# Optimization experiments

Hardware: AMD Instinct MI355X
Metric: run time of the kernel (lower is better)

## Reference

```python
import jax, jax.numpy as jnp
import numpy as np

B, K, N, F = 32, 4, 512, 128


def setup_inputs() -> dict:
    key = jax.random.key(0)
    k1, k2, k3, k4 = jax.random.split(key, 4)
    H = jax.random.normal(k1, (B, N, F), dtype=jnp.float32)
    E = jax.random.uniform(k2, (B, K, N, N), dtype=jnp.float32)
    # xavier_normal_ equivalents
    rw_std = float(np.sqrt(2.0 / (F + F * K)))  # torch xavier treats last dims
    RW = jax.random.normal(k3, (F, F, K), dtype=jnp.float32) * rw_std
    sw_std = float(np.sqrt(2.0 / (F + F)))
    SW = jax.random.normal(k4, (F, F), dtype=jnp.float32) * sw_std
    return {"H": H, "E": E, "RW": RW, "SW": SW}


def reference(H, E, RW, SW):
    # D = 1 / sum over (k, i) of (E + I)  -> [b, n]
    n = E.shape[2]
    D = 1.0 / (E + jnp.eye(n, dtype=E.dtype)).sum(axis=(1, 2))  # [b, n]
    # relational aggregation: sum_{k,j,m} E[b,k,i,j] H[b,j,m] RW[m,f,k] -> [b,i,f]
    rel = jnp.einsum('bkij,bjm,mfk->bif', E, H, RW)
    self_term = jnp.einsum('bjf,fl->bjl', H, SW)
    return jax.nn.sigmoid(D[:, :, None] * rel + self_term)
```

## Files before the change

### kernel.cpp

```cpp
#include <hip/hip_runtime.h>
#include <hip/hip_bf16.h>

#define B_ 32
#define K_ 4
#define N_ 512
#define F_ 128

typedef __attribute__((ext_vector_type(8))) short short8;
typedef __attribute__((ext_vector_type(4))) short short4v;
typedef __attribute__((ext_vector_type(4))) float float4v;

__device__ __forceinline__ unsigned short f2bf(float x) {
    unsigned int u = __builtin_bit_cast(unsigned int, x);
    u += 0x7FFFu + ((u >> 16) & 1u);
    return (unsigned short)(u >> 16);
}

__device__ __forceinline__ short8 pack8(float4v a, float4v b) {
    short8 r;
    r[0] = (short)f2bf(a[0]); r[1] = (short)f2bf(a[1]);
    r[2] = (short)f2bf(a[2]); r[3] = (short)f2bf(a[3]);
    r[4] = (short)f2bf(b[0]); r[5] = (short)f2bf(b[1]);
    r[6] = (short)f2bf(b[2]); r[7] = (short)f2bf(b[3]);
    return r;
}

__global__ void k0_weights(const float* __restrict__ RW, const float* __restrict__ SW,
                           unsigned short* __restrict__ Wt, unsigned short* __restrict__ SWt) {
    int r = blockIdx.x;
    int m = threadIdx.x;
    if (r < 512) {
        int k = r >> 7, f = r & 127;
        Wt[r * F_ + m] = f2bf(RW[(m * F_ + f) * K_ + k]);
    } else {
        int l = r - 512;
        SWt[l * F_ + m] = f2bf(SW[m * F_ + l]);
    }
}

__global__ void __launch_bounds__(256)
k1v3_convert(const float* __restrict__ E, float* __restrict__ colsum,
             unsigned short* __restrict__ Ebf) {
    int bid = blockIdx.x;
    int b   = bid >> 6;
    int k   = (bid >> 4) & 3;
    int isl = bid & 15;
    int t   = threadIdx.x;
    int j8  = (t & 63) * 8;
    int r0  = isl * 32 + (t >> 6) * 8;

    const size_t base = ((size_t)((b * K_ + k) * N_ + r0)) * N_ + j8;
    const float* Ep = E + base;
    unsigned short* Op = Ebf + base;

    float4v va[8], vb[8];
#pragma unroll
    for (int r = 0; r < 4; ++r) {
        va[r] = *(const float4v*)(Ep + (size_t)r * N_);
        vb[r] = *(const float4v*)(Ep + (size_t)r * N_ + 4);
    }
#pragma unroll
    for (int r = 4; r < 8; ++r) {
        va[r] = *(const float4v*)(Ep + (size_t)r * N_);
        vb[r] = *(const float4v*)(Ep + (size_t)r * N_ + 4);
    }

    float cs[8];
#pragma unroll
    for (int e = 0; e < 8; ++e) cs[e] = 0.f;
#pragma unroll
    for (int r = 0; r < 8; ++r) {
        cs[0] += va[r][0]; cs[1] += va[r][1]; cs[2] += va[r][2]; cs[3] += va[r][3];
        cs[4] += vb[r][0]; cs[5] += vb[r][1]; cs[6] += vb[r][2]; cs[7] += vb[r][3];
        *(short8*)(Op + (size_t)r * N_) = pack8(va[r], vb[r]);
    }

    __shared__ float red[256][9];
#pragma unroll
    for (int e = 0; e < 8; ++e) red[t][e] = cs[e];
    __syncthreads();
    if (t < 64) {
#pragma unroll
        for (int e = 0; e < 8; ++e) {
            float s = red[t][e] + red[t + 64][e] + red[t + 128][e] + red[t + 192][e];
            atomicAdd(&colsum[b * N_ + t * 8 + e], s);
        }
    }
}

__global__ void __launch_bounds__(256)
k2v2_expand(const float* __restrict__ H, const unsigned short* __restrict__ Wt,
            unsigned short* __restrict__ Tt) {
    int bid = blockIdx.x;
    int b  = bid >> 5;
    int ct = (bid >> 2) & 7;
    int jt = bid & 3;
    int lane = threadIdx.x & 63;
    int wv   = threadIdx.x >> 6;
    int c0 = ct * 64 + wv * 16;
    int jbase = jt * 128;
    int lrow = lane & 15, lgrp = lane >> 4;

    float4v acc[8];
#pragma unroll
    for (int i = 0; i < 8; ++i) acc[i] = {0.f, 0.f, 0.f, 0.f};

#pragma unroll
    for (int ms = 0; ms < 4; ++ms) {
        int m0 = ms * 32;
        short8 a = *(const short8*)(Wt + (c0 + lrow) * F_ + m0 + lgrp * 8);
        float4v hv0[8], hv1[8];
#pragma unroll
        for (int cf = 0; cf < 8; ++cf) {
            const float* hp = H + ((size_t)b * N_ + jbase + cf * 16 + lrow) * F_ + m0 + lgrp * 8;
            hv0[cf] = *(const float4v*)hp;
            hv1[cf] = *(const float4v*)(hp + 4);
        }
#pragma unroll
        for (int cf = 0; cf < 8; ++cf) {
            short8 bb = pack8(hv0[cf], hv1[cf]);
            acc[cf] = __builtin_amdgcn_mfma_f32_16x16x32_bf16(a, bb, acc[cf], 0, 0, 0);
        }
    }
#pragma unroll
    for (int cf = 0; cf < 8; ++cf) {
#pragma unroll
        for (int r = 0; r < 4; ++r) {
            int c = c0 + lgrp * 4 + r;
            int j = jbase + cf * 16 + lrow;
            Tt[((size_t)b * 512 + c) * N_ + j] = f2bf(acc[cf][r]);
        }
    }
}

__global__ void __launch_bounds__(512)
k3v3_rel(const unsigned short* __restrict__ Ebf, const unsigned short* __restrict__ Tt,
         float* __restrict__ relP) {
    int bid = blockIdx.x;
    int b  = bid >> 5;
    int it = (bid >> 2) & 7;
    int jc = bid & 3;
    int lane = threadIdx.x & 63;
    int wv   = threadIdx.x >> 6;
    int i0 = it * 64 + (wv >> 1) * 16;
    int f0 = (wv & 1) * 64;
    int lrow = lane & 15, lgrp = lane >> 4;
    int jbase = jc * 128;

    float4v acc[4];
#pragma unroll
    for (int i = 0; i < 4; ++i) acc[i] = {0.f, 0.f, 0.f, 0.f};

    const unsigned short* Eb = Ebf + ((size_t)(b * K_) * N_ + (i0 + lrow)) * N_ + jbase + lgrp * 8;
    const unsigned short* Tb = Tt + ((size_t)b * 512 + f0 + lrow) * N_ + jbase + lgrp * 8;

#define EA(t) (const short8*)(Eb + ((t) >> 2) * 262144 + ((t) & 3) * 32)
#define TA(t, cf) (const short8*)(Tb + ((t) >> 2) * 65536 + (cf) * 8192 + ((t) & 3) * 32)

    short8 a0, b00, b01, b02, b03;
    short8 a1, b10, b11, b12, b13;
    a0 = *EA(0); b00 = *TA(0, 0); b01 = *TA(0, 1); b02 = *TA(0, 2); b03 = *TA(0, 3);

    for (int t = 0; t < 16; t += 2) {
        int t1 = t + 1;
        int t2 = (t + 2 < 16) ? t + 2 : 15;
        a1 = *EA(t1); b10 = *TA(t1, 0); b11 = *TA(t1, 1); b12 = *TA(t1, 2); b13 = *TA(t1, 3);
        acc[0] = __builtin_amdgcn_mfma_f32_16x16x32_bf16(a0, b00, acc[0], 0, 0, 0);
        acc[1] = __builtin_amdgcn_mfma_f32_16x16x32_bf16(a0, b01, acc[1], 0, 0, 0);
        acc[2] = __builtin_amdgcn_mfma_f32_16x16x32_bf16(a0, b02, acc[2], 0, 0, 0);
        acc[3] = __builtin_amdgcn_mfma_f32_16x16x32_bf16(a0, b03, acc[3], 0, 0, 0);
        a0 = *EA(t2); b00 = *TA(t2, 0); b01 = *TA(t2, 1); b02 = *TA(t2, 2); b03 = *TA(t2, 3);
        acc[0] = __builtin_amdgcn_mfma_f32_16x16x32_bf16(a1, b10, acc[0], 0, 0, 0);
        acc[1] = __builtin_amdgcn_mfma_f32_16x16x32_bf16(a1, b11, acc[1], 0, 0, 0);
        acc[2] = __builtin_amdgcn_mfma_f32_16x16x32_bf16(a1, b12, acc[2], 0, 0, 0);
        acc[3] = __builtin_amdgcn_mfma_f32_16x16x32_bf16(a1, b13, acc[3], 0, 0, 0);
    }
#undef EA
#undef TA

    float* dst = relP + (size_t)jc * (B_ * N_ * F_);
#pragma unroll
    for (int cf = 0; cf < 4; ++cf) {
#pragma unroll
        for (int r = 0; r < 4; ++r) {
            int i = i0 + lgrp * 4 + r;
            int f = f0 + cf * 16 + lrow;
            dst[((size_t)b * N_ + i) * F_ + f] = acc[cf][r];
        }
    }
}

__global__ void __launch_bounds__(512)
k4_epi(const float* __restrict__ relP, const float* __restrict__ H,
       const unsigned short* __restrict__ SWt, const float* __restrict__ colsum,
       float* __restrict__ out) {
    int bid = blockIdx.x;
    int b  = bid >> 3;
    int it = bid & 7;
    int lane = threadIdx.x & 63;
    int wv   = threadIdx.x >> 6;
    int i0 = it * 64 + (wv >> 1) * 16;
    int f0 = (wv & 1) * 64;
    int lrow = lane & 15, lgrp = lane >> 4;

    float4v accS[4];
#pragma unroll
    for (int i = 0; i < 4; ++i) accS[i] = {0.f, 0.f, 0.f, 0.f};

    const float* Hp = H + ((size_t)b * N_ + i0 + lrow) * F_;
#pragma unroll
    for (int ms = 0; ms < 4; ++ms) {
        int m0 = ms * 32;
        const float* hp = Hp + m0 + lgrp * 8;
        float4v h0 = *(const float4v*)hp;
        float4v h1 = *(const float4v*)(hp + 4);
        short8 a = pack8(h0, h1);
#pragma unroll
        for (int cf = 0; cf < 4; ++cf) {
            const unsigned short* sp = SWt + (f0 + cf * 16 + lrow) * F_ + m0 + lgrp * 8;
            short8 bb = *(const short8*)sp;
            accS[cf] = __builtin_amdgcn_mfma_f32_16x16x32_bf16(a, bb, accS[cf], 0, 0, 0);
        }
    }

    float Dv[4];
#pragma unroll
    for (int r = 0; r < 4; ++r) {
        int i = i0 + lgrp * 4 + r;
        Dv[r] = 1.0f / (colsum[b * N_ + i] + (float)K_);
    }
    const size_t S = (size_t)B_ * N_ * F_;
#pragma unroll
    for (int cf = 0; cf < 4; ++cf) {
#pragma unroll
        for (int r = 0; r < 4; ++r) {
            int i = i0 + lgrp * 4 + r;
            int f = f0 + cf * 16 + lrow;
            size_t idx = ((size_t)b * N_ + i) * F_ + f;
            float v = relP[idx] + relP[idx + S] + relP[idx + 2 * S] + relP[idx + 3 * S];
            float x = Dv[r] * v + accS[cf][r];
            out[idx] = 1.0f / (1.0f + __expf(-x));
        }
    }
}

__global__ void k1_colsum(const float* __restrict__ E, float* __restrict__ colsum) {
    int bid = blockIdx.x;
    int b   = bid >> 5;
    int jt  = (bid >> 4) & 1;
    int isl = bid & 15;
    int j   = jt * 256 + threadIdx.x;
    int i0  = isl * 32;
    float s0 = 0.f, s1 = 0.f, s2 = 0.f, s3 = 0.f;
#pragma unroll
    for (int k = 0; k < K_; ++k) {
        const float* p = E + ((size_t)((b * K_ + k) * N_ + i0)) * N_ + j;
#pragma unroll 4
        for (int ii = 0; ii < 32; ii += 4) {
            s0 += p[(ii + 0) * N_];
            s1 += p[(ii + 1) * N_];
            s2 += p[(ii + 2) * N_];
            s3 += p[(ii + 3) * N_];
        }
    }
    atomicAdd(&colsum[b * N_ + j], (s0 + s1) + (s2 + s3));
}

__global__ void __launch_bounds__(512)
k3_fuse(const float* __restrict__ E, const float* __restrict__ H,
        const unsigned short* __restrict__ Tt, const unsigned short* __restrict__ SWt,
        const float* __restrict__ colsum, float* __restrict__ out) {
    int bid = blockIdx.x;
    int b  = bid >> 3;
    int it = bid & 7;
    int lane = threadIdx.x & 63;
    int wv   = threadIdx.x >> 6;
    int i0 = it * 64 + (wv >> 1) * 16;
    int f0 = (wv & 1) * 64;
    int lrow = lane & 15, lgrp = lane >> 4;

    float4v accR[4], accS[4];
#pragma unroll
    for (int i = 0; i < 4; ++i) { accR[i] = {0.f, 0.f, 0.f, 0.f}; accS[i] = {0.f, 0.f, 0.f, 0.f}; }

    for (int k = 0; k < K_; ++k) {
        const float* Eb = E + ((size_t)((b * K_ + k) * N_ + i0 + lrow)) * N_;
        const unsigned short* Tb = Tt + ((size_t)b * 512 + k * 128 + f0) * N_;
#pragma unroll 2
        for (int js = 0; js < 16; ++js) {
            int j0 = js * 32;
            const float* ep = Eb + j0 + lgrp * 8;
            float4v e0 = *(const float4v*)ep;
            float4v e1 = *(const float4v*)(ep + 4);
            short8 a = pack8(e0, e1);
#pragma unroll
            for (int cf = 0; cf < 4; ++cf) {
                const unsigned short* tp = Tb + (size_t)(cf * 16 + lrow) * N_ + j0 + lgrp * 8;
                short8 bb = *(const short8*)tp;
                accR[cf] = __builtin_amdgcn_mfma_f32_16x16x32_bf16(a, bb, accR[cf], 0, 0, 0);
            }
        }
    }
    {
        const float* Hp = H + ((size_t)b * N_ + i0 + lrow) * F_;
#pragma unroll
        for (int ms = 0; ms < 4; ++ms) {
            int m0 = ms * 32;
            const float* hp = Hp + m0 + lgrp * 8;
            float4v h0 = *(const float4v*)hp;
            float4v h1 = *(const float4v*)(hp + 4);
            short8 a = pack8(h0, h1);
#pragma unroll
            for (int cf = 0; cf < 4; ++cf) {
                const unsigned short* sp = SWt + (f0 + cf * 16 + lrow) * F_ + m0 + lgrp * 8;
                short8 bb = *(const short8*)sp;
                accS[cf] = __builtin_amdgcn_mfma_f32_16x16x32_bf16(a, bb, accS[cf], 0, 0, 0);
            }
        }
    }
    float Dv[4];
#pragma unroll
    for (int r = 0; r < 4; ++r) {
        int i = i0 + lgrp * 4 + r;
        Dv[r] = 1.0f / (colsum[b * N_ + i] + (float)K_);
    }
#pragma unroll
    for (int cf = 0; cf < 4; ++cf) {
#pragma unroll
        for (int r = 0; r < 4; ++r) {
            int i = i0 + lgrp * 4 + r;
            int f = f0 + cf * 16 + lrow;
            float x = Dv[r] * accR[cf][r] + accS[cf][r];
            out[((size_t)b * N_ + i) * F_ + f] = 1.0f / (1.0f + __expf(-x));
        }
    }
}

extern "C" void kernel_launch(void* const* d_in, const int* in_sizes, int n_in,
                              void* d_out, int out_size, void* d_ws, size_t ws_size,
                              hipStream_t stream) {
    const float* H  = (const float*)d_in[0];
    const float* E  = (const float*)d_in[1];
    const float* RW = (const float*)d_in[2];
    const float* SW = (const float*)d_in[3];
    float* out = (float*)d_out;

    char* ws = (char*)d_ws;
    unsigned short* Wt  = (unsigned short*)(ws);
    unsigned short* SWt = (unsigned short*)(ws + 131072);
    float* colsum       = (float*)(ws + 163840);
    unsigned short* Tt  = (unsigned short*)(ws + 262144);
    unsigned short* Ebf = (unsigned short*)(ws + 17039360);
    float* relP         = (float*)(ws + 84148224);
    const size_t WS_NEED = 117702656ull;

    hipMemsetAsync(colsum, 0, B_ * N_ * sizeof(float), stream);
    k0_weights<<<640, 128, 0, stream>>>(RW, SW, Wt, SWt);

    if (ws_size >= WS_NEED) {
        k1v3_convert<<<2048, 256, 0, stream>>>(E, colsum, Ebf);
        k2v2_expand<<<1024, 256, 0, stream>>>(H, Wt, Tt);
        k3v3_rel<<<1024, 512, 0, stream>>>(Ebf, Tt, relP);
        k4_epi<<<256, 512, 0, stream>>>(relP, H, SWt, colsum, out);
    } else {
        k1_colsum<<<1024, 256, 0, stream>>>(E, colsum);
        k2v2_expand<<<1024, 256, 0, stream>>>(H, Wt, Tt);
        k3_fuse<<<256, 512, 0, stream>>>(E, H, Tt, SWt, colsum, out);
    }
}
```

Baseline: 342.2 us.

## Fuse E bf16 conversion and column sums into relational GEMM kernel

Removes the separate pass that converts E to bf16 and writes it to workspace. The GEMM kernel now loads fp32 E directly, packs it to bf16 in registers, and computes the column sums with wave shuffles plus atomics. This drops a full bf16 write and re-read of the large E tensor. The loop order now iterates k fastest. The trade-offs are fp32 loads twice as wide feeding the MFMA loop and extra VALU work in half the waves.

Measured after the change: 326.4 us. -4.6%, faster.

```diff
diff --git a/kernel.cpp b/kernel.cpp
--- a/kernel.cpp
+++ b/kernel.cpp
@@ -7,7 +7,6 @@
 #define F_ 128
 
 typedef __attribute__((ext_vector_type(8))) short short8;
-typedef __attribute__((ext_vector_type(4))) short short4v;
 typedef __attribute__((ext_vector_type(4))) float float4v;
 
 __device__ __forceinline__ unsigned short f2bf(float x) {
@@ -39,56 +38,6 @@
 }
 
 __global__ void __launch_bounds__(256)
-k1v3_convert(const float* __restrict__ E, float* __restrict__ colsum,
-             unsigned short* __restrict__ Ebf) {
-    int bid = blockIdx.x;
-    int b   = bid >> 6;
-    int k   = (bid >> 4) & 3;
-    int isl = bid & 15;
-    int t   = threadIdx.x;
-    int j8  = (t & 63) * 8;
-    int r0  = isl * 32 + (t >> 6) * 8;
-
-    const size_t base = ((size_t)((b * K_ + k) * N_ + r0)) * N_ + j8;
-    const float* Ep = E + base;
-    unsigned short* Op = Ebf + base;
-
-    float4v va[8], vb[8];
-#pragma unroll
-    for (int r = 0; r < 4; ++r) {
-        va[r] = *(const float4v*)(Ep + (size_t)r * N_);
-        vb[r] = *(const float4v*)(Ep + (size_t)r * N_ + 4);
-    }
-#pragma unroll
-    for (int r = 4; r < 8; ++r) {
-        va[r] = *(const float4v*)(Ep + (size_t)r * N_);
-        vb[r] = *(const float4v*)(Ep + (size_t)r * N_ + 4);
-    }
-
-    float cs[8];
-#pragma unroll
-    for (int e = 0; e < 8; ++e) cs[e] = 0.f;
-#pragma unroll
-    for (int r = 0; r < 8; ++r) {
-        cs[0] += va[r][0]; cs[1] += va[r][1]; cs[2] += va[r][2]; cs[3] += va[r][3];
-        cs[4] += vb[r][0]; cs[5] += vb[r][1]; cs[6] += vb[r][2]; cs[7] += vb[r][3];
-        *(short8*)(Op + (size_t)r * N_) = pack8(va[r], vb[r]);
-    }
-
-    __shared__ float red[256][9];
-#pragma unroll
-    for (int e = 0; e < 8; ++e) red[t][e] = cs[e];
-    __syncthreads();
-    if (t < 64) {
-#pragma unroll
-        for (int e = 0; e < 8; ++e) {
-            float s = red[t][e] + red[t + 64][e] + red[t + 128][e] + red[t + 192][e];
-            atomicAdd(&colsum[b * N_ + t * 8 + e], s);
-        }
-    }
-}
-
-__global__ void __launch_bounds__(256)
 k2v2_expand(const float* __restrict__ H, const unsigned short* __restrict__ Wt,
             unsigned short* __restrict__ Tt) {
     int bid = blockIdx.x;
@@ -134,8 +83,8 @@
 }
 
 __global__ void __launch_bounds__(512)
-k3v3_rel(const unsigned short* __restrict__ Ebf, const unsigned short* __restrict__ Tt,
-         float* __restrict__ relP) {
+kA_fused(const float* __restrict__ E, const unsigned short* __restrict__ Tt,
+         float* __restrict__ colsum, float* __restrict__ relP) {
     int bid = blockIdx.x;
     int b  = bid >> 5;
     int it = (bid >> 2) & 7;
@@ -146,36 +95,79 @@
     int f0 = (wv & 1) * 64;
     int lrow = lane & 15, lgrp = lane >> 4;
     int jbase = jc * 128;
+    bool do_cs = (wv & 1) == 0;
 
     float4v acc[4];
 #pragma unroll
     for (int i = 0; i < 4; ++i) acc[i] = {0.f, 0.f, 0.f, 0.f};
-
-    const unsigned short* Eb = Ebf + ((size_t)(b * K_) * N_ + (i0 + lrow)) * N_ + jbase + lgrp * 8;
+    float cs[8];
+#pragma unroll
+    for (int e = 0; e < 8; ++e) cs[e] = 0.f;
+
+    const float* Eb = E + ((size_t)(b * K_) * N_ + (i0 + lrow)) * N_ + jbase + lgrp * 8;
     const unsigned short* Tb = Tt + ((size_t)b * 512 + f0 + lrow) * N_ + jbase + lgrp * 8;
 
-#define EA(t) (const short8*)(Eb + ((t) >> 2) * 262144 + ((t) & 3) * 32)
-#define TA(t, cf) (const short8*)(Tb + ((t) >> 2) * 65536 + (cf) * 8192 + ((t) & 3) * 32)
-
-    short8 a0, b00, b01, b02, b03;
-    short8 a1, b10, b11, b12, b13;
-    a0 = *EA(0); b00 = *TA(0, 0); b01 = *TA(0, 1); b02 = *TA(0, 2); b03 = *TA(0, 3);
-
+#define EA0(t) (const float4v*)(Eb + ((t) & 3) * 262144 + ((t) >> 2) * 32)
+#define EA1(t) (const float4v*)(Eb + ((t) & 3) * 262144 + ((t) >> 2) * 32 + 4)
+#define TA(t, cf) (const short8*)(Tb + ((t) & 3) * 65536 + (cf) * 8192 + ((t) >> 2) * 32)
+
+    float4v ea0, eb0, ea1, eb1;
+    short8 t00, t01, t02, t03, t10, t11, t12, t13;
+    ea0 = *EA0(0); eb0 = *EA1(0);
+    t00 = *TA(0, 0); t01 = *TA(0, 1); t02 = *TA(0, 2); t03 = *TA(0, 3);
+
+#pragma unroll
     for (int t = 0; t < 16; t += 2) {
         int t1 = t + 1;
         int t2 = (t + 2 < 16) ? t + 2 : 15;
-        a1 = *EA(t1); b10 = *TA(t1, 0); b11 = *TA(t1, 1); b12 = *TA(t1, 2); b13 = *TA(t1, 3);
-        acc[0] = __builtin_amdgcn_mfma_f32_16x16x32_bf16(a0, b00, acc[0], 0, 0, 0);
-        acc[1] = __builtin_amdgcn_mfma_f32_16x16x32_bf16(a0, b01, acc[1], 0, 0, 0);
-        acc[2] = __builtin_amdgcn_mfma_f32_16x16x32_bf16(a0, b02, acc[2], 0, 0, 0);
-        acc[3] = __builtin_amdgcn_mfma_f32_16x16x32_bf16(a0, b03, acc[3], 0, 0, 0);
-        a0 = *EA(t2); b00 = *TA(t2, 0); b01 = *TA(t2, 1); b02 = *TA(t2, 2); b03 = *TA(t2, 3);
-        acc[0] = __builtin_amdgcn_mfma_f32_16x16x32_bf16(a1, b10, acc[0], 0, 0, 0);
-        acc[1] = __builtin_amdgcn_mfma_f32_16x16x32_bf16(a1, b11, acc[1], 0, 0, 0);
-        acc[2] = __builtin_amdgcn_mfma_f32_16x16x32_bf16(a1, b12, acc[2], 0, 0, 0);
-        acc[3] = __builtin_amdgcn_mfma_f32_16x16x32_bf16(a1, b13, acc[3], 0, 0, 0);
-    }
-#undef EA
+        ea1 = *EA0(t1); eb1 = *EA1(t1);
+        t10 = *TA(t1, 0); t11 = *TA(t1, 1); t12 = *TA(t1, 2); t13 = *TA(t1, 3);
+        {
+            short8 a = pack8(ea0, eb0);
+            acc[0] = __builtin_amdgcn_mfma_f32_16x16x32_bf16(a, t00, acc[0], 0, 0, 0);
+            acc[1] = __builtin_amdgcn_mfma_f32_16x16x32_bf16(a, t01, acc[1], 0, 0, 0);
+            acc[2] = __builtin_amdgcn_mfma_f32_16x16x32_bf16(a, t02, acc[2], 0, 0, 0);
+            acc[3] = __builtin_amdgcn_mfma_f32_16x16x32_bf16(a, t03, acc[3], 0, 0, 0);
+            if (do_cs) {
+                cs[0] += ea0[0]; cs[1] += ea0[1]; cs[2] += ea0[2]; cs[3] += ea0[3];
+                cs[4] += eb0[0]; cs[5] += eb0[1]; cs[6] += eb0[2]; cs[7] += eb0[3];
+            }
+        }
+        ea0 = *EA0(t2); eb0 = *EA1(t2);
+        t00 = *TA(t2, 0); t01 = *TA(t2, 1); t02 = *TA(t2, 2); t03 = *TA(t2, 3);
+        {
+            short8 a = pack8(ea1, eb1);
+            acc[0] = __builtin_amdgcn_mfma_f32_16x16x32_bf16(a, t10, acc[0], 0, 0, 0);
+            acc[1] = __builtin_amdgcn_mfma_f32_16x16x32_bf16(a, t11, acc[1], 0, 0, 0);
+            acc[2] = __builtin_amdgcn_mfma_f32_16x16x32_bf16(a, t12, acc[2], 0, 0, 0);
+            acc[3] = __builtin_amdgcn_mfma_f32_16x16x32_bf16(a, t13, acc[3], 0, 0, 0);
+            if (do_cs) {
+                cs[0] += ea1[0]; cs[1] += ea1[1]; cs[2] += ea1[2]; cs[3] += ea1[3];
+                cs[4] += eb1[0]; cs[5] += eb1[1]; cs[6] += eb1[2]; cs[7] += eb1[3];
+            }
+        }
+        if (((t1) & 3) == 3) {
+            int js = t1 >> 2;
+            if (do_cs) {
+#pragma unroll
+                for (int e = 0; e < 8; ++e) {
+                    cs[e] += __shfl_xor(cs[e], 1);
+                    cs[e] += __shfl_xor(cs[e], 2);
+                    cs[e] += __shfl_xor(cs[e], 4);
+                    cs[e] += __shfl_xor(cs[e], 8);
+                }
+                if (lrow == 0) {
+#pragma unroll
+                    for (int e = 0; e < 8; ++e)
+                        atomicAdd(&colsum[b * N_ + jbase + js * 32 + lgrp * 8 + e], cs[e]);
+                }
+#pragma unroll
+                for (int e = 0; e < 8; ++e) cs[e] = 0.f;
+            }
+        }
+    }
+#undef EA0
+#undef EA1
 #undef TA
 
     float* dst = relP + (size_t)jc * (B_ * N_ * F_);
@@ -350,21 +342,18 @@
     unsigned short* SWt = (unsigned short*)(ws + 131072);
     float* colsum       = (float*)(ws + 163840);
     unsigned short* Tt  = (unsigned short*)(ws + 262144);
-    unsigned short* Ebf = (unsigned short*)(ws + 17039360);
-    float* relP         = (float*)(ws + 84148224);
-    const size_t WS_NEED = 117702656ull;
+    float* relP         = (float*)(ws + 17039360);
+    const size_t WS_NEED = 50593792ull;
 
     hipMemsetAsync(colsum, 0, B_ * N_ * sizeof(float), stream);
     k0_weights<<<640, 128, 0, stream>>>(RW, SW, Wt, SWt);
+    k2v2_expand<<<1024, 256, 0, stream>>>(H, Wt, Tt);
 
     if (ws_size >= WS_NEED) {
-        k1v3_convert<<<2048, 256, 0, stream>>>(E, colsum, Ebf);
-        k2v2_expand<<<1024, 256, 0, stream>>>(H, Wt, Tt);
-        k3v3_rel<<<1024, 512, 0, stream>>>(Ebf, Tt, relP);
+        kA_fused<<<1024, 512, 0, stream>>>(E, Tt, colsum, relP);
         k4_epi<<<256, 512, 0, stream>>>(relP, H, SWt, colsum, out);
     } else {
         k1_colsum<<<1024, 256, 0, stream>>>(E, colsum);
-        k2v2_expand<<<1024, 256, 0, stream>>>(H, Wt, Tt);
         k3_fuse<<<256, 512, 0, stream>>>(E, H, Tt, SWt, colsum, out);
     }
 }
```

## Stage rel GEMM tiles through LDS with async global-to-LDS loads and split-j reduction

Applied to the files above, without the earlier changes.

The relational GEMM kernel now stages E and T tiles into double-buffered, XOR-swizzled shared memory using global_load_lds, so that loads are shared across waves instead of each wave loading from global memory separately. The j dimension is split two ways instead of four, which halves the partial-sum buffer and the epilogue's reads of it. The E conversion kernel is also rewritten as a finer-grained streaming kernel with one float8 per thread and a shared-memory column reduction. The tradeoffs are fewer blocks in the GEMM (512 instead of 1024), a barrier on every k-step, and many more small blocks in the conversion kernel.

Result: faster. 283.4 us (-17.2%).

```diff
diff --git a/kernel.cpp b/kernel.cpp
--- a/kernel.cpp
+++ b/kernel.cpp
@@ -7,7 +7,6 @@
 #define F_ 128
 
 typedef __attribute__((ext_vector_type(8))) short short8;
-typedef __attribute__((ext_vector_type(4))) short short4v;
 typedef __attribute__((ext_vector_type(4))) float float4v;
 
 __device__ __forceinline__ unsigned short f2bf(float x) {
@@ -23,6 +22,12 @@
     r[4] = (short)f2bf(b[0]); r[5] = (short)f2bf(b[1]);
     r[6] = (short)f2bf(b[2]); r[7] = (short)f2bf(b[3]);
     return r;
+}
+
+__device__ __forceinline__ void gl16(const void* g, void* l) {
+    __builtin_amdgcn_global_load_lds(
+        (const __attribute__((address_space(1))) void*)g,
+        (__attribute__((address_space(3))) void*)l, 16, 0, 0);
 }
 
 __global__ void k0_weights(const float* __restrict__ RW, const float* __restrict__ SW,
@@ -39,52 +44,33 @@
 }
 
 __global__ void __launch_bounds__(256)
-k1v3_convert(const float* __restrict__ E, float* __restrict__ colsum,
-             unsigned short* __restrict__ Ebf) {
-    int bid = blockIdx.x;
-    int b   = bid >> 6;
-    int k   = (bid >> 4) & 3;
-    int isl = bid & 15;
-    int t   = threadIdx.x;
-    int j8  = (t & 63) * 8;
-    int r0  = isl * 32 + (t >> 6) * 8;
-
-    const size_t base = ((size_t)((b * K_ + k) * N_ + r0)) * N_ + j8;
-    const float* Ep = E + base;
-    unsigned short* Op = Ebf + base;
-
-    float4v va[8], vb[8];
-#pragma unroll
-    for (int r = 0; r < 4; ++r) {
-        va[r] = *(const float4v*)(Ep + (size_t)r * N_);
-        vb[r] = *(const float4v*)(Ep + (size_t)r * N_ + 4);
-    }
-#pragma unroll
-    for (int r = 4; r < 8; ++r) {
-        va[r] = *(const float4v*)(Ep + (size_t)r * N_);
-        vb[r] = *(const float4v*)(Ep + (size_t)r * N_ + 4);
-    }
-
-    float cs[8];
-#pragma unroll
-    for (int e = 0; e < 8; ++e) cs[e] = 0.f;
-#pragma unroll
-    for (int r = 0; r < 8; ++r) {
-        cs[0] += va[r][0]; cs[1] += va[r][1]; cs[2] += va[r][2]; cs[3] += va[r][3];
-        cs[4] += vb[r][0]; cs[5] += vb[r][1]; cs[6] += vb[r][2]; cs[7] += vb[r][3];
-        *(short8*)(Op + (size_t)r * N_) = pack8(va[r], vb[r]);
-    }
-
-    __shared__ float red[256][9];
-#pragma unroll
-    for (int e = 0; e < 8; ++e) red[t][e] = cs[e];
+kS_stream(const float* __restrict__ E, float* __restrict__ colsum,
+          unsigned short* __restrict__ Ebf) {
+    int bid = blockIdx.x;
+    int b     = bid >> 9;
+    int k     = (bid >> 7) & 3;
+    int rslab = (bid >> 3) & 15;
+    int cslab = bid & 7;
+    int t = threadIdx.x;
+    int rl = t >> 3;
+    int cl = (t & 7) * 8;
+
+    size_t base = ((size_t)((b * K_ + k) * N_ + rslab * 32 + rl)) * N_ + cslab * 64 + cl;
+    float4v v0 = *(const float4v*)(E + base);
+    float4v v1 = *(const float4v*)(E + base + 4);
+    *(short8*)(Ebf + base) = pack8(v0, v1);
+
+    __shared__ float red[32][65];
+    red[rl][cl + 0] = v0[0]; red[rl][cl + 1] = v0[1];
+    red[rl][cl + 2] = v0[2]; red[rl][cl + 3] = v0[3];
+    red[rl][cl + 4] = v1[0]; red[rl][cl + 5] = v1[1];
+    red[rl][cl + 6] = v1[2]; red[rl][cl + 7] = v1[3];
     __syncthreads();
     if (t < 64) {
-#pragma unroll
-        for (int e = 0; e < 8; ++e) {
-            float s = red[t][e] + red[t + 64][e] + red[t + 128][e] + red[t + 192][e];
-            atomicAdd(&colsum[b * N_ + t * 8 + e], s);
-        }
+        float s = 0.f;
+#pragma unroll
+        for (int r = 0; r < 32; ++r) s += red[r][t];
+        atomicAdd(&colsum[b * N_ + cslab * 64 + t], s);
     }
 }
 
@@ -134,66 +120,88 @@
 }
 
 __global__ void __launch_bounds__(512)
-k3v3_rel(const unsigned short* __restrict__ Ebf, const unsigned short* __restrict__ Tt,
-         float* __restrict__ relP) {
-    int bid = blockIdx.x;
-    int b  = bid >> 5;
-    int it = (bid >> 2) & 7;
-    int jc = bid & 3;
-    int lane = threadIdx.x & 63;
-    int wv   = threadIdx.x >> 6;
-    int i0 = it * 64 + (wv >> 1) * 16;
-    int f0 = (wv & 1) * 64;
+kB_rel(const unsigned short* __restrict__ Ebf, const unsigned short* __restrict__ Tt,
+       float* __restrict__ relP) {
+    __shared__ char smem[24576];
+    int bid = blockIdx.x;
+    int b  = bid >> 4;
+    int it = (bid >> 1) & 7;
+    int jc = bid & 1;
+    int tid = threadIdx.x;
+    int lane = tid & 63, wv = tid >> 6;
     int lrow = lane & 15, lgrp = lane >> 4;
-    int jbase = jc * 128;
+    int isub = wv >> 1, fh = wv & 1;
 
     float4v acc[4];
 #pragma unroll
     for (int i = 0; i < 4; ++i) acc[i] = {0.f, 0.f, 0.f, 0.f};
 
-    const unsigned short* Eb = Ebf + ((size_t)(b * K_) * N_ + (i0 + lrow)) * N_ + jbase + lgrp * 8;
-    const unsigned short* Tb = Tt + ((size_t)b * 512 + f0 + lrow) * N_ + jbase + lgrp * 8;
-
-#define EA(t) (const short8*)(Eb + ((t) >> 2) * 262144 + ((t) & 3) * 32)
-#define TA(t, cf) (const short8*)(Tb + ((t) >> 2) * 65536 + (cf) * 8192 + ((t) & 3) * 32)
-
-    short8 a0, b00, b01, b02, b03;
-    short8 a1, b10, b11, b12, b13;
-    a0 = *EA(0); b00 = *TA(0, 0); b01 = *TA(0, 1); b02 = *TA(0, 2); b03 = *TA(0, 3);
-
-    for (int t = 0; t < 16; t += 2) {
-        int t1 = t + 1;
-        int t2 = (t + 2 < 16) ? t + 2 : 15;
-        a1 = *EA(t1); b10 = *TA(t1, 0); b11 = *TA(t1, 1); b12 = *TA(t1, 2); b13 = *TA(t1, 3);
-        acc[0] = __builtin_amdgcn_mfma_f32_16x16x32_bf16(a0, b00, acc[0], 0, 0, 0);
-        acc[1] = __builtin_amdgcn_mfma_f32_16x16x32_bf16(a0, b01, acc[1], 0, 0, 0);
-        acc[2] = __builtin_amdgcn_mfma_f32_16x16x32_bf16(a0, b02, acc[2], 0, 0, 0);
-        acc[3] = __builtin_amdgcn_mfma_f32_16x16x32_bf16(a0, b03, acc[3], 0, 0, 0);
-        a0 = *EA(t2); b00 = *TA(t2, 0); b01 = *TA(t2, 1); b02 = *TA(t2, 2); b03 = *TA(t2, 3);
-        acc[0] = __builtin_amdgcn_mfma_f32_16x16x32_bf16(a1, b10, acc[0], 0, 0, 0);
-        acc[1] = __builtin_amdgcn_mfma_f32_16x16x32_bf16(a1, b11, acc[1], 0, 0, 0);
-        acc[2] = __builtin_amdgcn_mfma_f32_16x16x32_bf16(a1, b12, acc[2], 0, 0, 0);
-        acc[3] = __builtin_amdgcn_mfma_f32_16x16x32_bf16(a1, b13, acc[3], 0, 0, 0);
-    }
-#undef EA
-#undef TA
+    int slotT = wv * 64 + lane;
+    int rT = slotT >> 2, gT = slotT & 3;
+    int colT = (gT ^ (rT & 3)) * 8;
+    int slotE = (wv & 3) * 64 + lane;
+    int rE = slotE >> 2, gE = slotE & 3;
+    int colE = (gE ^ (rE & 3)) * 8;
+
+    const unsigned short* Tbase = Tt + ((size_t)(b * 512 + rT)) * N_ + jc * 256 + colT;
+    const unsigned short* Ebase = Ebf + ((size_t)(b * K_ * N_) + it * 64 + rE) * N_ + jc * 256 + colE;
+
+#define STAGE(bufoff, kk, js)                                                        \
+    {                                                                                \
+        gl16(Tbase + (size_t)(kk) * (128 * N_) + (js) * 32,                          \
+             smem + (bufoff) + 4096 + wv * 1024);                                    \
+        if (wv < 4)                                                                  \
+            gl16(Ebase + (size_t)(kk) * (N_ * N_) + (js) * 32,                       \
+                 smem + (bufoff) + (wv & 3) * 1024);                                 \
+    }
+
+    STAGE(0, 0, 0);
+    __syncthreads();
+
+    int rA = isub * 16 + lrow;
+    int eoffA = rA * 64 + ((lgrp ^ (rA & 3)) << 4);
+    int toff0 = (fh * 64 + 0 * 16 + lrow) * 64 + ((lgrp ^ (lrow & 3)) << 4);
+    int toff1 = (fh * 64 + 1 * 16 + lrow) * 64 + ((lgrp ^ (lrow & 3)) << 4);
+    int toff2 = (fh * 64 + 2 * 16 + lrow) * 64 + ((lgrp ^ (lrow & 3)) << 4);
+    int toff3 = (fh * 64 + 3 * 16 + lrow) * 64 + ((lgrp ^ (lrow & 3)) << 4);
+
+    int cur = 0;
+    for (int t = 0; t < 32; ++t) {
+        int nxt = cur ^ 12288;
+        if (t + 1 < 32) {
+            int k1 = (t + 1) & 3, js1 = (t + 1) >> 2;
+            STAGE(nxt, k1, js1);
+        }
+        short8 a  = *(const short8*)(smem + cur + eoffA);
+        short8 b0 = *(const short8*)(smem + cur + 4096 + toff0);
+        short8 b1 = *(const short8*)(smem + cur + 4096 + toff1);
+        short8 b2 = *(const short8*)(smem + cur + 4096 + toff2);
+        short8 b3 = *(const short8*)(smem + cur + 4096 + toff3);
+        acc[0] = __builtin_amdgcn_mfma_f32_16x16x32_bf16(a, b0, acc[0], 0, 0, 0);
+        acc[1] = __builtin_amdgcn_mfma_f32_16x16x32_bf16(a, b1, acc[1], 0, 0, 0);
+        acc[2] = __builtin_amdgcn_mfma_f32_16x16x32_bf16(a, b2, acc[2], 0, 0, 0);
+        acc[3] = __builtin_amdgcn_mfma_f32_16x16x32_bf16(a, b3, acc[3], 0, 0, 0);
+        __syncthreads();
+        cur = nxt;
+    }
+#undef STAGE
 
     float* dst = relP + (size_t)jc * (B_ * N_ * F_);
 #pragma unroll
     for (int cf = 0; cf < 4; ++cf) {
 #pragma unroll
         for (int r = 0; r < 4; ++r) {
-            int i = i0 + lgrp * 4 + r;
-            int f = f0 + cf * 16 + lrow;
+            int i = it * 64 + isub * 16 + lgrp * 4 + r;
+            int f = fh * 64 + cf * 16 + lrow;
             dst[((size_t)b * N_ + i) * F_ + f] = acc[cf][r];
         }
     }
 }
 
 __global__ void __launch_bounds__(512)
-k4_epi(const float* __restrict__ relP, const float* __restrict__ H,
-       const unsigned short* __restrict__ SWt, const float* __restrict__ colsum,
-       float* __restrict__ out) {
+k4_epi2(const float* __restrict__ relP, const float* __restrict__ H,
+        const unsigned short* __restrict__ SWt, const float* __restrict__ colsum,
+        float* __restrict__ out) {
     int bid = blockIdx.x;
     int b  = bid >> 3;
     int it = bid & 7;
@@ -237,7 +245,7 @@
             int i = i0 + lgrp * 4 + r;
             int f = f0 + cf * 16 + lrow;
             size_t idx = ((size_t)b * N_ + i) * F_ + f;
-            float v = relP[idx] + relP[idx + S] + relP[idx + 2 * S] + relP[idx + 3 * S];
+            float v = relP[idx] + relP[idx + S];
             float x = Dv[r] * v + accS[cf][r];
             out[idx] = 1.0f / (1.0f + __expf(-x));
         }
@@ -352,16 +360,16 @@
     unsigned short* Tt  = (unsigned short*)(ws + 262144);
     unsigned short* Ebf = (unsigned short*)(ws + 17039360);
     float* relP         = (float*)(ws + 84148224);
-    const size_t WS_NEED = 117702656ull;
+    const size_t WS_NEED = 100925440ull;
 
     hipMemsetAsync(colsum, 0, B_ * N_ * sizeof(float), stream);
     k0_weights<<<640, 128, 0, stream>>>(RW, SW, Wt, SWt);
 
     if (ws_size >= WS_NEED) {
-        k1v3_convert<<<2048, 256, 0, stream>>>(E, colsum, Ebf);
+        kS_stream<<<16384, 256, 0, stream>>>(E, colsum, Ebf);
         k2v2_expand<<<1024, 256, 0, stream>>>(H, Wt, Tt);
-        k3v3_rel<<<1024, 512, 0, stream>>>(Ebf, Tt, relP);
-        k4_epi<<<256, 512, 0, stream>>>(relP, H, SWt, colsum, out);
+        kB_rel<<<512, 512, 0, stream>>>(Ebf, Tt, relP);
+        k4_epi2<<<256, 512, 0, stream>>>(relP, H, SWt, colsum, out);
     } else {
         k1_colsum<<<1024, 256, 0, stream>>>(E, colsum);
         k2v2_expand<<<1024, 256, 0, stream>>>(H, Wt, Tt);
```
